# Kernel optimization log

Measured on AMD Instinct MI355X. Metric: run time of the kernel, lower is better.

The kernel has to match this reference:

```python
import jax, jax.numpy as jnp
import numpy as np


def graph_conv(x, W, b, src, dst, n_nodes):
    """DGL GraphConv, norm='both', activation=relu.
    Pre-scale by out-degree^-1/2 of src, project (in>out so project first),
    sum-aggregate over edges, post-scale by in-degree^-1/2 of dst."""
    ones = jnp.ones(src.shape[0], dtype=x.dtype)
    deg_out = jax.ops.segment_sum(ones, src, num_segments=n_nodes)
    deg_in = jax.ops.segment_sum(ones, dst, num_segments=n_nodes)
    norm_src = jnp.clip(deg_out, 1.0, None) ** -0.5  # [N]
    norm_dst = jnp.clip(deg_in, 1.0, None) ** -0.5   # [N]
    h = x * norm_src[:, None]
    h = h @ W  # project first since in_feats > out_feats
    # message passing: gather src features, scatter-add into dst
    agg = jax.ops.segment_sum(h[src], dst, num_segments=n_nodes)  # [N, out]
    agg = agg * norm_dst[:, None]
    return jax.nn.relu(agg + b)


def setup_inputs() -> dict:
    key = jax.random.key(0)
    ks = jax.random.split(key, 6)
    N, E, D_IN, D_HID = 50000, 800000, 1024, 256
    x = jax.random.normal(ks[0], (N, D_IN), dtype=jnp.float32)
    src = jax.random.randint(ks[1], (E,), 0, N)
    dst = jax.random.randint(ks[2], (E,), 0, N)
    # Glorot-style init for weights
    W1 = jax.random.normal(ks[3], (D_IN, D_HID), dtype=jnp.float32) * (1.0 / np.sqrt(D_IN))
    b1 = jnp.zeros((D_HID,), dtype=jnp.float32)
    W2 = jax.random.normal(ks[4], (D_HID, 1), dtype=jnp.float32) * (1.0 / np.sqrt(D_HID))
    b2 = jnp.zeros((1,), dtype=jnp.float32)
    return {"x": x, "src": src, "dst": dst, "W1": W1, "b1": b1, "W2": W2, "b2": b2, "n_nodes": N}


def reference(x, src, dst, W1, b1, W2, b2, n_nodes):
    h = graph_conv(x, W1, b1, src, dst, n_nodes)   # [N, 256]
    out = graph_conv(h, W2, b2, src, dst, n_nodes)  # [N, 1]
    return out
```

## Files before the change

kernel.cpp:

```cpp
#include <hip/hip_runtime.h>
#include <hip/hip_bf16.h>

typedef __attribute__((ext_vector_type(8))) short bf16x8;
typedef __attribute__((ext_vector_type(4))) float f32x4;

static __device__ __forceinline__ short f2bf(float f) {
    unsigned u = __float_as_uint(f);
    unsigned r = (u + 0x7FFFu + ((u >> 16) & 1u)) >> 16;
    return (short)(unsigned short)r;
}
static __device__ __forceinline__ float bf2f(short s) {
    return __uint_as_float(((unsigned)(unsigned short)s) << 16);
}

static __device__ __forceinline__ void gload16(const void* g, void* l) {
    __builtin_amdgcn_global_load_lds((const __attribute__((address_space(1))) unsigned int*)g,
                                     (__attribute__((address_space(3))) unsigned int*)l, 16, 0, 0);
}

static __device__ __forceinline__ void wg_barrier() {
    asm volatile("" ::: "memory");
    __builtin_amdgcn_s_barrier();
    asm volatile("" ::: "memory");
}

static __device__ __forceinline__ bf16x8 cvt8(const f32x4 lo, const f32x4 hi) {
    __hip_bfloat162 p0 = __float22bfloat162_rn(make_float2(lo[0], lo[1]));
    __hip_bfloat162 p1 = __float22bfloat162_rn(make_float2(lo[2], lo[3]));
    __hip_bfloat162 p2 = __float22bfloat162_rn(make_float2(hi[0], hi[1]));
    __hip_bfloat162 p3 = __float22bfloat162_rn(make_float2(hi[2], hi[3]));
    short2 s0 = *(short2*)&p0, s1 = *(short2*)&p1, s2 = *(short2*)&p2, s3 = *(short2*)&p3;
    bf16x8 r = {s0.x, s0.y, s1.x, s1.y, s2.x, s2.y, s3.x, s3.y};
    return r;
}

__global__ void deg_kernel(const int* __restrict__ src, const int* __restrict__ dst,
                           int* __restrict__ deg_out, int* __restrict__ deg_in, int E) {
    int e = blockIdx.x * blockDim.x + threadIdx.x;
    if (e < E) {
        atomicAdd(&deg_out[src[e]], 1);
        atomicAdd(&deg_in[dst[e]], 1);
    }
}

__global__ void scan_part1(const int* __restrict__ deg, int* __restrict__ bsum, int N) {
    __shared__ int red[256];
    int i = blockIdx.x * 256 + threadIdx.x;
    red[threadIdx.x] = (i < N) ? deg[i] : 0;
    __syncthreads();
    for (int off = 128; off > 0; off >>= 1) {
        if (threadIdx.x < off) red[threadIdx.x] += red[threadIdx.x + off];
        __syncthreads();
    }
    if (threadIdx.x == 0) bsum[blockIdx.x] = red[0];
}

__global__ void scan_part2(const int* __restrict__ bsum, int* __restrict__ bsum_ex, int NB,
                           int* __restrict__ offsets, int N, int E) {
    __shared__ int s[256];
    int t = threadIdx.x;
    int v = (t < NB) ? bsum[t] : 0;
    s[t] = v;
    __syncthreads();
    for (int off = 1; off < 256; off <<= 1) {
        int u = (t >= off) ? s[t - off] : 0;
        __syncthreads();
        s[t] += u;
        __syncthreads();
    }
    bsum_ex[t] = s[t] - v;
    if (t == 0) offsets[N] = E;
}

__global__ void scan_part3(const int* __restrict__ deg_in, const int* __restrict__ deg_out,
                           const int* __restrict__ bsum_ex, int* __restrict__ offsets,
                           float* __restrict__ ns, float* __restrict__ nd, int N) {
    __shared__ int s[256];
    int t = threadIdx.x, i = blockIdx.x * 256 + t;
    int v = (i < N) ? deg_in[i] : 0;
    s[t] = v;
    __syncthreads();
    for (int off = 1; off < 256; off <<= 1) {
        int u = (t >= off) ? s[t - off] : 0;
        __syncthreads();
        s[t] += u;
        __syncthreads();
    }
    if (i < N) {
        offsets[i] = bsum_ex[blockIdx.x] + s[t] - v;
        ns[i] = rsqrtf((float)max(deg_out[i], 1));
        nd[i] = rsqrtf((float)max(v, 1));
    }
}

__global__ void scatter_kernel(const int* __restrict__ src, const int* __restrict__ dst,
                               const int* __restrict__ offsets, int* __restrict__ cursor,
                               int* __restrict__ bucket, int E) {
    int e = blockIdx.x * blockDim.x + threadIdx.x;
    if (e < E) {
        int d = dst[e];
        int p = atomicAdd(&cursor[d], 1);
        bucket[offsets[d] + p] = src[e];
    }
}

__global__ __launch_bounds__(1024) void transpose_w1(const float* __restrict__ W1,
                                                     short* __restrict__ Wt) {
    __shared__ short tile[32][33];
    int k0 = blockIdx.x * 32, n0 = blockIdx.y * 32;
    int tx = threadIdx.x & 31, ty = threadIdx.x >> 5;
    tile[ty][tx] = f2bf(W1[(size_t)(k0 + ty) * 256 + (n0 + tx)]);
    __syncthreads();
    Wt[(size_t)(n0 + ty) * 1024 + (k0 + tx)] = tile[tx][ty];
}

#define BM 128
#define BN 256
#define BK 32
#define NKT 32
#define CSTR 264

union SMem {
    short B[2][BN * BK];
    short C[BM * CSTR];
};

__global__ __launch_bounds__(256, 2) void gemm1_kernel(const float* __restrict__ x,
                                                       const short* __restrict__ Wt,
                                                       const float* __restrict__ norm_src,
                                                       short* __restrict__ hb, int M) {
    __shared__ __align__(16) SMem sm;
    __shared__ float ns_lds[BM];
    const int tid  = threadIdx.x;
    const int lane = tid & 63;
    const int wave = tid >> 6;
    const int quad = lane >> 4;
    const int mrow = lane & 15;
    const int wm = (wave >> 1) * 64;
    const int wn = (wave & 1) * 128;
    const int bm = blockIdx.x * BM;

    if (tid < BM) ns_lds[tid] = norm_src[min(bm + tid, M - 1)];

    f32x4 acc[4][8] = {};

    const float* aptr[4];
#pragma unroll
    for (int mi = 0; mi < 4; mi++) {
        int row = min(bm + wm + mi * 16 + mrow, M - 1);
        aptr[mi] = x + (size_t)row * 1024 + quad * 8;
    }

    const int bL_r = lane >> 2;
    const int bL_c = (lane & 3) ^ ((lane >> 3) & 3);

    auto stageB = [&](int buf, int k0) {
#pragma unroll
        for (int i = 0; i < 4; i++) {
            int nbase = wave * 64 + i * 16;
            int n = nbase + bL_r;
            gload16(Wt + (size_t)n * 1024 + k0 + bL_c * 8, &sm.B[buf][nbase * 32]);
        }
    };

    f32x4 aLo[4], aHi[4];
    bf16x8 af[4];

    stageB(0, 0);
#pragma unroll
    for (int mi = 0; mi < 4; mi++) {
        aLo[mi] = *(const f32x4*)(aptr[mi]);
        aHi[mi] = *(const f32x4*)(aptr[mi] + 4);
    }
    stageB(1, BK);
    asm volatile("s_waitcnt vmcnt(4)" ::: "memory");
#pragma unroll
    for (int mi = 0; mi < 4; mi++) af[mi] = cvt8(aLo[mi], aHi[mi]);
    wg_barrier();

    int cur = 0;
    for (int t = 0; t < NKT; t++) {
        if (t + 1 < NKT) {
            int k = (t + 1) * BK;
#pragma unroll
            for (int mi = 0; mi < 4; mi++) {
                aLo[mi] = *(const f32x4*)(aptr[mi] + k);
                aHi[mi] = *(const f32x4*)(aptr[mi] + k + 4);
            }
        }

        bf16x8 bfr[8];
#pragma unroll
        for (int ni = 0; ni < 8; ni++) {
            int n = wn + ni * 16 + mrow;
            bfr[ni] = *(const bf16x8*)&sm.B[cur][n * 32 + ((quad ^ ((mrow >> 1) & 3)) * 8)];
        }
#pragma unroll
        for (int mi = 0; mi < 4; mi++)
#pragma unroll
            for (int ni = 0; ni < 8; ni++)
                acc[mi][ni] = __builtin_amdgcn_mfma_f32_16x16x32_bf16(af[mi], bfr[ni], acc[mi][ni], 0, 0, 0);

        wg_barrier();

        if (t + 2 < NKT) {
            stageB(cur, (t + 2) * BK);
            asm volatile("s_waitcnt vmcnt(4)" ::: "memory");
        } else {
            asm volatile("s_waitcnt vmcnt(0)" ::: "memory");
        }
        if (t + 1 < NKT) {
#pragma unroll
            for (int mi = 0; mi < 4; mi++) af[mi] = cvt8(aLo[mi], aHi[mi]);
        }
        wg_barrier();
        cur ^= 1;
    }

#pragma unroll
    for (int mi = 0; mi < 4; mi++) {
#pragma unroll
        for (int reg = 0; reg < 4; reg++) {
            int row = wm + mi * 16 + quad * 4 + reg;
            float nsv = ns_lds[row];
#pragma unroll
            for (int ni = 0; ni < 8; ni++) {
                int col = wn + ni * 16 + mrow;
                sm.C[row * CSTR + col] = f2bf(acc[mi][ni][reg] * nsv);
            }
        }
    }
    __syncthreads();
#pragma unroll
    for (int j = 0; j < 16; j++) {
        int row = wave * 2 + (lane >> 5) + j * 8;
        int chunk = lane & 31;
        if (bm + row < M) {
            int4 v = *(const int4*)&sm.C[row * CSTR + chunk * 8];
            *(int4*)(hb + (size_t)(bm + row) * 256 + chunk * 8) = v;
        }
    }
}

__global__ __launch_bounds__(256) void agg1_kernel(const short* __restrict__ hb,
                                                   const int* __restrict__ bucket,
                                                   const int* __restrict__ offsets,
                                                   const float* __restrict__ norm_dst,
                                                   const float* __restrict__ norm_src,
                                                   const float* __restrict__ b1,
                                                   const float* __restrict__ W2,
                                                   float* __restrict__ z, int N) {
    int wave = threadIdx.x >> 6;
    int lane = threadIdx.x & 63;
    int half = lane >> 5;
    int col8 = lane & 31;
    int node = blockIdx.x * 4 + wave;
    if (node >= N) return;
    int beg = offsets[node], end = offsets[node + 1];
    float a[8] = {0.f, 0.f, 0.f, 0.f, 0.f, 0.f, 0.f, 0.f};
    int e = beg;
    for (; e + 8 <= end; e += 8) {
        int s0 = bucket[e + 0 + half];
        int s1 = bucket[e + 2 + half];
        int s2 = bucket[e + 4 + half];
        int s3 = bucket[e + 6 + half];
        bf16x8 v0 = *(const bf16x8*)(hb + (size_t)s0 * 256 + col8 * 8);
        bf16x8 v1 = *(const bf16x8*)(hb + (size_t)s1 * 256 + col8 * 8);
        bf16x8 v2 = *(const bf16x8*)(hb + (size_t)s2 * 256 + col8 * 8);
        bf16x8 v3 = *(const bf16x8*)(hb + (size_t)s3 * 256 + col8 * 8);
#pragma unroll
        for (int j = 0; j < 8; j++)
            a[j] += bf2f(v0[j]) + bf2f(v1[j]) + bf2f(v2[j]) + bf2f(v3[j]);
    }
    for (; e + 2 <= end; e += 2) {
        int s0 = bucket[e + half];
        bf16x8 v0 = *(const bf16x8*)(hb + (size_t)s0 * 256 + col8 * 8);
#pragma unroll
        for (int j = 0; j < 8; j++) a[j] += bf2f(v0[j]);
    }
    if (e < end && half == 0) {
        int s0 = bucket[e];
        bf16x8 v0 = *(const bf16x8*)(hb + (size_t)s0 * 256 + col8 * 8);
#pragma unroll
        for (int j = 0; j < 8; j++) a[j] += bf2f(v0[j]);
    }
#pragma unroll
    for (int j = 0; j < 8; j++) a[j] += __shfl_xor(a[j], 32, 64);

    float nd = norm_dst[node];
    float4 b_lo = *(const float4*)(b1 + col8 * 8);
    float4 b_hi = *(const float4*)(b1 + col8 * 8 + 4);
    float4 w_lo = *(const float4*)(W2 + col8 * 8);
    float4 w_hi = *(const float4*)(W2 + col8 * 8 + 4);
    float p = 0.f;
    p += fmaxf(a[0] * nd + b_lo.x, 0.f) * w_lo.x;
    p += fmaxf(a[1] * nd + b_lo.y, 0.f) * w_lo.y;
    p += fmaxf(a[2] * nd + b_lo.z, 0.f) * w_lo.z;
    p += fmaxf(a[3] * nd + b_lo.w, 0.f) * w_lo.w;
    p += fmaxf(a[4] * nd + b_hi.x, 0.f) * w_hi.x;
    p += fmaxf(a[5] * nd + b_hi.y, 0.f) * w_hi.y;
    p += fmaxf(a[6] * nd + b_hi.z, 0.f) * w_hi.z;
    p += fmaxf(a[7] * nd + b_hi.w, 0.f) * w_hi.w;
#pragma unroll
    for (int off = 16; off > 0; off >>= 1) p += __shfl_xor(p, off, 64);
    if (lane == 0) z[node] = p * norm_src[node];
}

__global__ void agg2_kernel(const float* __restrict__ z, const int* __restrict__ bucket,
                            const int* __restrict__ offsets, const float* __restrict__ norm_dst,
                            const float* __restrict__ b2, float* __restrict__ out, int N) {
    int i = blockIdx.x * blockDim.x + threadIdx.x;
    if (i >= N) return;
    int beg = offsets[i], end = offsets[i + 1];
    float s = 0.f;
    for (int e = beg; e < end; e++) s += z[bucket[e]];
    out[i] = fmaxf(s * norm_dst[i] + b2[0], 0.f);
}

extern "C" void kernel_launch(void* const* d_in, const int* in_sizes, int n_in,
                              void* d_out, int out_size, void* d_ws, size_t ws_size,
                              hipStream_t stream) {
    const int D_HID = in_sizes[4];
    const int D_IN  = in_sizes[3] / D_HID;
    const int N     = in_sizes[0] / D_IN;
    const int E     = in_sizes[1];

    const float* x   = (const float*)d_in[0];
    const int*   src = (const int*)d_in[1];
    const int*   dst = (const int*)d_in[2];
    const float* W1  = (const float*)d_in[3];
    const float* b1  = (const float*)d_in[4];
    const float* W2  = (const float*)d_in[5];
    const float* b2  = (const float*)d_in[6];
    float* out = (float*)d_out;

    char* p = (char*)d_ws;
    auto alloc = [&](size_t bytes) {
        void* r = (void*)p;
        p += (bytes + 255) & ~(size_t)255;
        return r;
    };
    int*   deg_out  = (int*)alloc((size_t)N * 4);
    int*   deg_in   = (int*)alloc((size_t)N * 4);
    int*   cursor   = (int*)alloc((size_t)N * 4);
    float* norm_src = (float*)alloc((size_t)N * 4);
    float* norm_dst = (float*)alloc((size_t)N * 4);
    int*   offsets  = (int*)alloc((size_t)(N + 1) * 4);
    int*   bucket   = (int*)alloc((size_t)E * 4);
    short* Wt       = (short*)alloc((size_t)D_IN * D_HID * 2);
    short* hb       = (short*)alloc((size_t)N * D_HID * 2);
    float* z        = (float*)alloc((size_t)N * 4);
    int*   bsum     = (int*)alloc(256 * 4);
    int*   bsum_ex  = (int*)alloc(256 * 4);

    const int NB = (N + 255) / 256;

    size_t degpad = ((size_t)N * 4 + 255) & ~(size_t)255;
    hipMemsetAsync(deg_out, 0, degpad * 2 + (size_t)N * 4, stream);

    deg_kernel<<<(E + 255) / 256, 256, 0, stream>>>(src, dst, deg_out, deg_in, E);
    scan_part1<<<NB, 256, 0, stream>>>(deg_in, bsum, N);
    scan_part2<<<1, 256, 0, stream>>>(bsum, bsum_ex, NB, offsets, N, E);
    scan_part3<<<NB, 256, 0, stream>>>(deg_in, deg_out, bsum_ex, offsets, norm_src, norm_dst, N);
    scatter_kernel<<<(E + 255) / 256, 256, 0, stream>>>(src, dst, offsets, cursor, bucket, E);
    transpose_w1<<<dim3(D_IN / 32, D_HID / 32), 1024, 0, stream>>>(W1, Wt);
    gemm1_kernel<<<dim3((N + BM - 1) / BM), 256, 0, stream>>>(x, Wt, norm_src, hb, N);
    agg1_kernel<<<(N + 3) / 4, 256, 0, stream>>>(hb, bucket, offsets, norm_dst, norm_src, b1, W2, z, N);
    agg2_kernel<<<(N + 255) / 256, 256, 0, stream>>>(z, bucket, offsets, norm_dst, b2, out, N);
}
```

Before: 512.6 us.

## Triple-buffer GEMM B tiles with one barrier per step; deepen aggregation unroll

The GEMM moves from a double-buffered to a triple-buffered LDS ring for the weight tiles. This lets the next-next tile be issued before the MFMAs and drops one workgroup barrier per k-step. The fp32-to-bf16 conversion of the A fragments now runs before the wait, so it overlaps outstanding loads. The aggregation kernel gains a 16-edge unrolled loop with 8 independent gathers in flight to raise memory-level parallelism. The cost is more LDS for B, though the union with the C staging buffer may absorb it, plus higher register pressure in both kernels.

```diff
diff --git a/kernel.cpp b/kernel.cpp
--- a/kernel.cpp
+++ b/kernel.cpp
@@ -121,7 +121,7 @@
 #define CSTR 264
 
 union SMem {
-    short B[2][BN * BK];
+    short B[3][BN * BK];
     short C[BM * CSTR];
 };
 
@@ -173,9 +173,9 @@
         aHi[mi] = *(const f32x4*)(aptr[mi] + 4);
     }
     stageB(1, BK);
+#pragma unroll
+    for (int mi = 0; mi < 4; mi++) af[mi] = cvt8(aLo[mi], aHi[mi]);
     asm volatile("s_waitcnt vmcnt(4)" ::: "memory");
-#pragma unroll
-    for (int mi = 0; mi < 4; mi++) af[mi] = cvt8(aLo[mi], aHi[mi]);
     wg_barrier();
 
     int cur = 0;
@@ -188,6 +188,10 @@
                 aHi[mi] = *(const f32x4*)(aptr[mi] + k + 4);
             }
         }
+        if (t + 2 < NKT) {
+            int nb = cur + 2; if (nb >= 3) nb -= 3;
+            stageB(nb, (t + 2) * BK);
+        }
 
         bf16x8 bfr[8];
 #pragma unroll
@@ -201,20 +205,17 @@
             for (int ni = 0; ni < 8; ni++)
                 acc[mi][ni] = __builtin_amdgcn_mfma_f32_16x16x32_bf16(af[mi], bfr[ni], acc[mi][ni], 0, 0, 0);
 
-        wg_barrier();
-
+        if (t + 1 < NKT) {
+#pragma unroll
+            for (int mi = 0; mi < 4; mi++) af[mi] = cvt8(aLo[mi], aHi[mi]);
+        }
         if (t + 2 < NKT) {
-            stageB(cur, (t + 2) * BK);
             asm volatile("s_waitcnt vmcnt(4)" ::: "memory");
         } else {
             asm volatile("s_waitcnt vmcnt(0)" ::: "memory");
         }
-        if (t + 1 < NKT) {
-#pragma unroll
-            for (int mi = 0; mi < 4; mi++) af[mi] = cvt8(aLo[mi], aHi[mi]);
-        }
         wg_barrier();
-        cur ^= 1;
+        cur = (cur == 2) ? 0 : cur + 1;
     }
 
 #pragma unroll
@@ -259,18 +260,29 @@
     int beg = offsets[node], end = offsets[node + 1];
     float a[8] = {0.f, 0.f, 0.f, 0.f, 0.f, 0.f, 0.f, 0.f};
     int e = beg;
+    for (; e + 16 <= end; e += 16) {
+        bf16x8 v[8];
+#pragma unroll
+        for (int i = 0; i < 8; i++) {
+            int s = bucket[e + 2 * i + half];
+            v[i] = *(const bf16x8*)(hb + (size_t)s * 256 + col8 * 8);
+        }
+#pragma unroll
+        for (int i = 0; i < 8; i++)
+#pragma unroll
+            for (int j = 0; j < 8; j++) a[j] += bf2f(v[i][j]);
+    }
     for (; e + 8 <= end; e += 8) {
-        int s0 = bucket[e + 0 + half];
-        int s1 = bucket[e + 2 + half];
-        int s2 = bucket[e + 4 + half];
-        int s3 = bucket[e + 6 + half];
-        bf16x8 v0 = *(const bf16x8*)(hb + (size_t)s0 * 256 + col8 * 8);
-        bf16x8 v1 = *(const bf16x8*)(hb + (size_t)s1 * 256 + col8 * 8);
-        bf16x8 v2 = *(const bf16x8*)(hb + (size_t)s2 * 256 + col8 * 8);
-        bf16x8 v3 = *(const bf16x8*)(hb + (size_t)s3 * 256 + col8 * 8);
-#pragma unroll
-        for (int j = 0; j < 8; j++)
-            a[j] += bf2f(v0[j]) + bf2f(v1[j]) + bf2f(v2[j]) + bf2f(v3[j]);
+        bf16x8 v[4];
+#pragma unroll
+        for (int i = 0; i < 4; i++) {
+            int s = bucket[e + 2 * i + half];
+            v[i] = *(const bf16x8*)(hb + (size_t)s * 256 + col8 * 8);
+        }
+#pragma unroll
+        for (int i = 0; i < 4; i++)
+#pragma unroll
+            for (int j = 0; j < 8; j++) a[j] += bf2f(v[i][j]);
     }
     for (; e + 2 <= end; e += 2) {
         int s0 = bucket[e + half];
```

Result: no change. 515.1 us (+0.5%).
